# Optimization experiments

Hardware: AMD Instinct MI355X
Metric: run time of the kernel (lower is better)

Reference implementation:

```python
import jax, jax.numpy as jnp
import numpy as np

EMB = 1024
HEADS = 16
HEADSIZE = EMB // HEADS
EPS = 1e-5  # torch LayerNorm default


def _layernorm(x, g, b):
    # normalize over last dim (headsize)
    m = jnp.mean(x, axis=-1, keepdims=True)
    v = jnp.mean((x - m) ** 2, axis=-1, keepdims=True)
    return (x - m) * jax.lax.rsqrt(v + EPS) * g + b


def setup_inputs() -> dict:
    key = jax.random.key(0)
    ks = jax.random.split(key, 6)
    B, T = 4, 2048
    s = 1.0 / np.sqrt(EMB)  # ~ torch Linear init scale
    return {
        "x": jax.random.normal(ks[0], (B, T, EMB), dtype=jnp.float32),
        "Wk": jax.random.normal(ks[1], (EMB, EMB), dtype=jnp.float32) * s,
        "Wq": jax.random.normal(ks[2], (EMB, EMB), dtype=jnp.float32) * s,
        "Wv": jax.random.normal(ks[3], (EMB, EMB), dtype=jnp.float32) * s,
        "Wo": jax.random.normal(ks[4], (EMB, EMB), dtype=jnp.float32) * s,
        "bo": jnp.zeros((EMB,), dtype=jnp.float32),
        "kln_g": jnp.ones((HEADSIZE,), dtype=jnp.float32),
        "kln_b": jnp.zeros((HEADSIZE,), dtype=jnp.float32),
        "qln_g": jnp.ones((HEADSIZE,), dtype=jnp.float32),
        "qln_b": jnp.zeros((HEADSIZE,), dtype=jnp.float32),
    }


def reference(x, Wk, Wq, Wv, Wo, bo, kln_g, kln_b, qln_g, qln_b):
    B, T, E = x.shape
    # projections (torch Linear: y = x @ W.T), split into heads
    k = jnp.einsum("bte,fe->btf", x, Wk).reshape(B, T, HEADS, HEADSIZE)
    q = jnp.einsum("bte,fe->btf", x, Wq).reshape(B, T, HEADS, HEADSIZE)
    v = jnp.einsum("bte,fe->btf", x, Wv).reshape(B, T, HEADS, HEADSIZE)
    # optional per-head layernorm on keys/queries (kqnorm=True)
    k = _layernorm(k, kln_g, kln_b)
    q = _layernorm(q, qln_g, qln_b)
    # note: original scales by emb**-1/4 on each of q and k (total 1/sqrt(emb))
    scale = E ** (-0.25)
    q = q * scale
    k = k * scale
    # full [B, H, T, T] score matrix (faithful to bmm implementation)
    dot = jnp.einsum("bihd,bjhd->bhij", q, k)
    # causal mask: j > i set to -inf (mask_diagonal=False -> offset=1)
    causal = jnp.triu(jnp.ones((T, T), dtype=bool), k=1)
    dot = jnp.where(causal, -jnp.inf, dot)
    att = jax.nn.softmax(dot, axis=-1)
    out = jnp.einsum("bhij,bjhd->bihd", att, v).reshape(B, T, E)
    return jnp.einsum("bte,fe->btf", out, Wo) + bo
```

## Files before the change

### kernel.cpp

```cpp
#include <hip/hip_runtime.h>
#include <hip/hip_bf16.h>
#include <cstdint>

#define EMB 1024
#define HEADS 16
#define HD 64
#define BATCH 4
#define SEQ 2048
#define BT (BATCH*SEQ)
#define LNEPS 1e-5f
#define QK_SCALE 0.17677669529663687f
#define LOG2E 1.4426950408889634f

typedef __bf16 bf16;
typedef __bf16 bf16x8 __attribute__((ext_vector_type(8)));
typedef __bf16 bf16x4 __attribute__((ext_vector_type(4)));
typedef float  f32x4  __attribute__((ext_vector_type(4)));
typedef short  s16x4  __attribute__((ext_vector_type(4)));

typedef const __attribute__((address_space(1))) void* gas_ptr;
typedef __attribute__((address_space(3))) void*       las_ptr;

__device__ __forceinline__ void gld_lds16(const void* g, void* l) {
  __builtin_amdgcn_global_load_lds((gas_ptr)g, (las_ptr)l, 16, 0, 0);
}

__device__ __forceinline__ f32x4 mfma_pv(bf16x4 a, bf16x4 b, f32x4 c) {
  return __builtin_amdgcn_mfma_f32_16x16x16bf16_1k(
      __builtin_bit_cast(s16x4, a), __builtin_bit_cast(s16x4, b), c, 0, 0, 0);
}

__global__ void cvt_f32_bf16(const float* __restrict__ src, bf16* __restrict__ dst, int n4) {
  int i = blockIdx.x * blockDim.x + threadIdx.x;
  if (i >= n4) return;
  float4 f = reinterpret_cast<const float4*>(src)[i];
  bf16x4 o = { (bf16)f.x, (bf16)f.y, (bf16)f.z, (bf16)f.w };
  reinterpret_cast<bf16x4*>(dst)[i] = o;
}

__global__ void cvt_w4(const float* __restrict__ w0, const float* __restrict__ w1,
                       const float* __restrict__ w2, const float* __restrict__ w3,
                       bf16* __restrict__ dst) {
  int i = blockIdx.x * blockDim.x + threadIdx.x;
  int sel = i >> 18;
  int j = i & 262143;
  const float* s = (sel == 0) ? w0 : (sel == 1) ? w1 : (sel == 2) ? w2 : w3;
  float4 f = reinterpret_cast<const float4*>(s)[j];
  bf16x4 o = { (bf16)f.x, (bf16)f.y, (bf16)f.z, (bf16)f.w };
  reinterpret_cast<bf16x4*>(dst)[i] = o;
}

template<int OUTF32>
__global__ __launch_bounds__(256, 2) void gemm_bt(
    const bf16* __restrict__ A, const bf16* __restrict__ Bm,
    bf16* __restrict__ Cb, float* __restrict__ Cf, const float* __restrict__ bias,
    int M, int N, int K)
{
  __shared__ __align__(16) bf16 As[128 * 32];
  __shared__ __align__(16) bf16 Bs[128 * 32];

  const int t    = threadIdx.x;
  const int lane = t & 63;
  const int wave = t >> 6;
  const int q    = lane >> 4;
  const int ln   = lane & 15;
  const int m0   = blockIdx.y * 128;
  const int n0   = blockIdx.x * 128;
  const int wm   = (wave >> 1) * 64;
  const int wn   = (wave & 1) * 64;

  const int r0 = t >> 2;
  const int c0 = (t & 3) << 3;

  f32x4 zero4 = {0.f, 0.f, 0.f, 0.f};
  f32x4 acc[4][4];
#pragma unroll
  for (int i = 0; i < 4; i++)
#pragma unroll
    for (int j = 0; j < 4; j++) acc[i][j] = zero4;

  for (int k0 = 0; k0 < K; k0 += 32) {
    __syncthreads();
    const bf16* ga = A  + (size_t)(m0 + r0) * K + k0 + c0;
    const bf16* gb = Bm + (size_t)(n0 + r0) * K + k0 + c0;
    gld_lds16(ga,                  &As[t * 8]);
    gld_lds16(ga + (size_t)64 * K, &As[t * 8 + 2048]);
    gld_lds16(gb,                  &Bs[t * 8]);
    gld_lds16(gb + (size_t)64 * K, &Bs[t * 8 + 2048]);
    __syncthreads();

    bf16x8 af[4], bfr[4];
#pragma unroll
    for (int mi = 0; mi < 4; mi++)
      af[mi] = *reinterpret_cast<const bf16x8*>(&As[(wm + mi * 16 + ln) * 32 + q * 8]);
#pragma unroll
    for (int ni = 0; ni < 4; ni++)
      bfr[ni] = *reinterpret_cast<const bf16x8*>(&Bs[(wn + ni * 16 + ln) * 32 + q * 8]);
#pragma unroll
    for (int mi = 0; mi < 4; mi++)
#pragma unroll
      for (int ni = 0; ni < 4; ni++)
        acc[mi][ni] = __builtin_amdgcn_mfma_f32_16x16x32_bf16(af[mi], bfr[ni], acc[mi][ni], 0, 0, 0);
  }

#pragma unroll
  for (int mi = 0; mi < 4; mi++) {
#pragma unroll
    for (int ni = 0; ni < 4; ni++) {
#pragma unroll
      for (int r = 0; r < 4; r++) {
        int row = m0 + wm + mi * 16 + q * 4 + r;
        int col = n0 + wn + ni * 16 + ln;
        float v = acc[mi][ni][r];
        if (OUTF32) Cf[(size_t)row * N + col] = v + bias[col];
        else        Cb[(size_t)row * N + col] = (bf16)v;
      }
    }
  }
}

__global__ void ln_kq(const bf16* __restrict__ kqv,
                      bf16* __restrict__ kn, bf16* __restrict__ qn,
                      const float* __restrict__ kg, const float* __restrict__ kb,
                      const float* __restrict__ qg, const float* __restrict__ qb,
                      float kscale, float qscale)
{
  const int t = threadIdx.x;
  const int lr = t & 7;
  const int row = blockIdx.x * 32 + (t >> 3);
  const int tok = row >> 4, h = row & 15;
  const size_t base = (size_t)tok * (3 * EMB) + h * HD + lr * 8;

  bf16x8 vk = *reinterpret_cast<const bf16x8*>(kqv + base);
  bf16x8 vq = *reinterpret_cast<const bf16x8*>(kqv + base + EMB);

  float fk[8], fq[8];
  float sk = 0.f, sq = 0.f, s2k = 0.f, s2q = 0.f;
#pragma unroll
  for (int e = 0; e < 8; e++) {
    fk[e] = (float)vk[e]; fq[e] = (float)vq[e];
    sk += fk[e]; sq += fq[e];
    s2k += fk[e] * fk[e]; s2q += fq[e] * fq[e];
  }
#pragma unroll
  for (int m = 1; m < 8; m <<= 1) {
    sk  += __shfl_xor(sk,  m, 64); sq  += __shfl_xor(sq,  m, 64);
    s2k += __shfl_xor(s2k, m, 64); s2q += __shfl_xor(s2q, m, 64);
  }
  float mk = sk * (1.f / 64.f), mq = sq * (1.f / 64.f);
  float rk = rsqrtf(s2k * (1.f / 64.f) - mk * mk + LNEPS) * kscale;
  float rq = rsqrtf(s2q * (1.f / 64.f) - mq * mq + LNEPS) * qscale;

  bf16x8 ok, oq;
#pragma unroll
  for (int e = 0; e < 8; e++) {
    float gk = kg[lr * 8 + e], bk2 = kb[lr * 8 + e];
    float gq = qg[lr * 8 + e], bq2 = qb[lr * 8 + e];
    ok[e] = (bf16)(((fk[e] - mk) * rk) * gk + bk2 * kscale);
    oq[e] = (bf16)(((fq[e] - mq) * rq) * gq + bq2 * qscale);
  }
  const int b = tok >> 11, tt = tok & 2047;
  const size_t o = ((size_t)(b * HEADS + h) * SEQ + tt) * HD + lr * 8;
  *reinterpret_cast<bf16x8*>(kn + o) = ok;
  *reinterpret_cast<bf16x8*>(qn + o) = oq;
}

__global__ void v_trans(const bf16* __restrict__ in, int ldin, bf16* __restrict__ out)
{
  __shared__ __align__(16) bf16 tile[64][72];
  int bh = blockIdx.y, jt = blockIdx.x;
  int b = bh >> 4, h = bh & 15;
  int t = threadIdx.x;
#pragma unroll
  for (int p = 0; p < 2; p++) {
    int rowj = p * 32 + (t >> 3);
    int cold = (t & 7) << 3;
    bf16x8 v = *reinterpret_cast<const bf16x8*>(
        &in[(size_t)(b * SEQ + jt * 64 + rowj) * ldin + h * HD + cold]);
    *reinterpret_cast<bf16x8*>(&tile[rowj][cold]) = v;
  }
  __syncthreads();
#pragma unroll
  for (int p = 0; p < 2; p++) {
    int rowd = p * 32 + (t >> 3);
    int colj = (t & 7) << 3;
    bf16x8 v;
#pragma unroll
    for (int jj = 0; jj < 8; jj++) v[jj] = tile[colj + jj][rowd];
    *reinterpret_cast<bf16x8*>(&out[((size_t)bh * HD + rowd) * SEQ + jt * 64 + colj]) = v;
  }
}

__global__ __launch_bounds__(256, 4) void attn(
    const bf16* __restrict__ Qn, const bf16* __restrict__ Kn, const bf16* __restrict__ Vt,
    bf16* __restrict__ O)
{
  __shared__ __align__(16) bf16 Ks[2][64 * 64];
  __shared__ __align__(16) bf16 Vs[2][64 * 64];

  const int id = blockIdx.x;
  const int bh = ((id >> 7) << 3) | (id & 7);
  const int bxi = (id >> 3) & 15;
  const int t = threadIdx.x, wave = t >> 6, lane = t & 63;
  const int q = lane >> 4, ln = lane & 15;
  const int b = bh >> 4, h = bh & 15;

  const int u0 = t * 8, u1 = t * 8 + 2048;
  const int kr0 = u0 >> 6, kc0 = ((u0 >> 3) & 7) ^ (kr0 & 7);
  const int kr1 = u1 >> 6, kc1 = ((u1 >> 3) & 7) ^ (kr1 & 7);
  const int vd0 = u0 >> 6, vc0 = ((u0 >> 3) & 7) ^ (vd0 & 7);
  const int vd1 = u1 >> 6, vc1 = ((u1 >> 3) & 7) ^ (vd1 & 7);
  const bf16* Kb = Kn + (size_t)bh * SEQ * HD;
  const bf16* Vb = Vt + (size_t)bh * HD * SEQ;

  f32x4 zero4 = {0.f, 0.f, 0.f, 0.f};

  for (int pass = 0; pass < 2; ++pass) {
    const int itile = pass ? (31 - bxi) : bxi;
    const int qbase = itile * 64 + wave * 16;

    const bf16* qp = Qn + ((size_t)bh * SEQ + qbase + ln) * HD + q * 8;
    bf16x8 qf0 = *reinterpret_cast<const bf16x8*>(qp);
    bf16x8 qf1 = *reinterpret_cast<const bf16x8*>(qp + 32);

    float lrow = 0.f;
    f32x4 oacc[4];
#pragma unroll
    for (int md = 0; md < 4; md++) oacc[md] = zero4;

    const int nj = itile + 1;

    __syncthreads();
    {
      gld_lds16(Kb + (size_t)kr0 * HD + kc0 * 8, &Ks[0][u0]);
      gld_lds16(Kb + (size_t)kr1 * HD + kc1 * 8, &Ks[0][u1]);
      gld_lds16(Vb + (size_t)vd0 * SEQ + vc0 * 8, &Vs[0][u0]);
      gld_lds16(Vb + (size_t)vd1 * SEQ + vc1 * 8, &Vs[0][u1]);
    }

    for (int jt = 0; jt < nj; ++jt) {
      const int buf = jt & 1;
      const int j0 = jt * 64;
      __syncthreads();
      if (jt + 1 < nj) {
        const int jn = j0 + 64;
        gld_lds16(Kb + (size_t)(jn + kr0) * HD + kc0 * 8, &Ks[buf ^ 1][u0]);
        gld_lds16(Kb + (size_t)(jn + kr1) * HD + kc1 * 8, &Ks[buf ^ 1][u1]);
        gld_lds16(Vb + (size_t)vd0 * SEQ + jn + vc0 * 8, &Vs[buf ^ 1][u0]);
        gld_lds16(Vb + (size_t)vd1 * SEQ + jn + vc1 * 8, &Vs[buf ^ 1][u1]);
      }

#pragma unroll
      for (int jb = 0; jb < 4; ++jb) {
        const int jslab = j0 + jb * 16;
        if (jslab <= qbase + 15) {
          const int rowj = jb * 16 + ln;
          bf16x8 kf0 = *reinterpret_cast<const bf16x8*>(
              &Ks[buf][rowj * 64 + ((q)     ^ (rowj & 7)) * 8]);
          bf16x8 kf1 = *reinterpret_cast<const bf16x8*>(
              &Ks[buf][rowj * 64 + ((4 + q) ^ (rowj & 7)) * 8]);
          f32x4 z = zero4;
          z = __builtin_amdgcn_mfma_f32_16x16x32_bf16(kf0, qf0, z, 0, 0, 0);
          z = __builtin_amdgcn_mfma_f32_16x16x32_bf16(kf1, qf1, z, 0, 0, 0);
          if (jslab + 15 > qbase) {
#pragma unroll
            for (int r = 0; r < 4; r++) {
              int jj = jslab + q * 4 + r;
              int ii = qbase + ln;
              if (jj > ii) z[r] = -1.0e30f;
            }
          }
          float p0 = exp2f(z[0]), p1 = exp2f(z[1]), p2 = exp2f(z[2]), p3 = exp2f(z[3]);
          lrow += (p0 + p1) + (p2 + p3);
          bf16x4 pk = { (bf16)p0, (bf16)p1, (bf16)p2, (bf16)p3 };

#pragma unroll
          for (int md = 0; md < 4; md++) {
            const int rowd = md * 16 + ln;
            const bf16* vp = &Vs[buf][rowd * 64 +
                (((jb * 2 + (q >> 1)) ^ (rowd & 7)) * 8) + (q & 1) * 4];
            bf16x4 vf = *reinterpret_cast<const bf16x4*>(vp);
            oacc[md] = mfma_pv(vf, pk, oacc[md]);
          }
        }
      }
    }

    float s = lrow;
    s += __shfl_xor(s, 16, 64);
    s += __shfl_xor(s, 32, 64);
    const float inv = 1.f / s;
    const int row = qbase + ln;
#pragma unroll
    for (int md = 0; md < 4; md++) {
      bf16x4 o4 = { (bf16)(oacc[md][0] * inv), (bf16)(oacc[md][1] * inv),
                    (bf16)(oacc[md][2] * inv), (bf16)(oacc[md][3] * inv) };
      int col = h * HD + md * 16 + q * 4;
      *reinterpret_cast<bf16x4*>(&O[(size_t)(b * SEQ + row) * EMB + col]) = o4;
    }
  }
}

extern "C" void kernel_launch(void* const* d_in, const int* in_sizes, int n_in,
                              void* d_out, int out_size, void* d_ws, size_t ws_size,
                              hipStream_t stream)
{
  const float* x   = (const float*)d_in[0];
  const float* Wk  = (const float*)d_in[1];
  const float* Wq  = (const float*)d_in[2];
  const float* Wv  = (const float*)d_in[3];
  const float* Wo  = (const float*)d_in[4];
  const float* bo  = (const float*)d_in[5];
  const float* klg = (const float*)d_in[6];
  const float* klb = (const float*)d_in[7];
  const float* qlg = (const float*)d_in[8];
  const float* qlb = (const float*)d_in[9];
  float* out = (float*)d_out;

  char* ws = (char*)d_ws;
  const size_t OFF_XB  = 0;
  const size_t OFF_WB  = OFF_XB  + (size_t)BT * EMB * 2;
  const size_t OFF_KQV = OFF_WB  + (size_t)4 * EMB * EMB * 2;
  const size_t OFF_KN  = OFF_KQV + (size_t)BT * 3 * EMB * 2;
  const size_t OFF_QN  = OFF_KN  + (size_t)BT * EMB * 2;
  const size_t OFF_VT  = OFF_QN  + (size_t)BT * EMB * 2;
  const size_t OFF_END = OFF_VT  + (size_t)BT * EMB * 2;
  if (ws_size < OFF_END) return;

  bf16* xb   = (bf16*)(ws + OFF_XB);
  bf16* wb   = (bf16*)(ws + OFF_WB);
  bf16* kqv  = (bf16*)(ws + OFF_KQV);
  bf16* kn   = (bf16*)(ws + OFF_KN);
  bf16* qn   = (bf16*)(ws + OFF_QN);
  bf16* vt   = (bf16*)(ws + OFF_VT);
  bf16* ob   = (bf16*)(ws + OFF_KQV);

  cvt_f32_bf16<<<(BT * EMB / 4) / 256, 256, 0, stream>>>(x, xb, BT * EMB / 4);
  cvt_w4<<<(4 * EMB * EMB / 4) / 256, 256, 0, stream>>>(Wk, Wq, Wv, Wo, wb);

  gemm_bt<0><<<dim3(3 * EMB / 128, BT / 128), 256, 0, stream>>>(
      xb, wb, kqv, (float*)nullptr, (const float*)nullptr, BT, 3 * EMB, EMB);

  ln_kq<<<BT * HEADS / 32, 256, 0, stream>>>(kqv, kn, qn, klg, klb, qlg, qlb,
                                             QK_SCALE * LOG2E, QK_SCALE);
  v_trans<<<dim3(SEQ / 64, BATCH * HEADS), 256, 0, stream>>>(kqv + 2 * EMB, 3 * EMB, vt);

  attn<<<dim3(16 * BATCH * HEADS), 256, 0, stream>>>(qn, kn, vt, ob);

  gemm_bt<1><<<dim3(EMB / 128, BT / 128), 256, 0, stream>>>(
      ob, wb + (size_t)3 * EMB * EMB, (bf16*)nullptr, out, bo, BT, EMB, EMB);
}
```

Measured before the change: 291.5 us.

## Process paired causal query tiles in one KV sweep sharing K/V loads

The attention kernel used to run two separate passes over the key/value tiles, one per paired query tile (bxi and 31-bxi). It now keeps both query tiles' accumulators live and streams K/V once up to the longer tile, computing the short tile only while jt <= iA. This roughly halves the K/V global-to-LDS traffic and barrier count for the short tile and gives more independent MFMA work per loaded tile. In exchange it holds more registers (two accumulator sets and two Q fragments), which could affect occupancy under launch_bounds(256,4).

Measured after the change: 288.9 us. Within noise of the previous version (-0.9%).

```diff
diff --git a/kernel.cpp b/kernel.cpp
--- a/kernel.cpp
+++ b/kernel.cpp
@@ -205,6 +205,11 @@
   const int q = lane >> 4, ln = lane & 15;
   const int b = bh >> 4, h = bh & 15;
 
+  const int iA = bxi;
+  const int iB = 31 - bxi;
+  const int qbaseA = iA * 64 + wave * 16;
+  const int qbaseB = iB * 64 + wave * 16;
+
   const int u0 = t * 8, u1 = t * 8 + 2048;
   const int kr0 = u0 >> 6, kc0 = ((u0 >> 3) & 7) ^ (kr0 & 7);
   const int kr1 = u1 >> 6, kc1 = ((u1 >> 3) & 7) ^ (kr1 & 7);
@@ -215,82 +220,95 @@
 
   f32x4 zero4 = {0.f, 0.f, 0.f, 0.f};
 
-  for (int pass = 0; pass < 2; ++pass) {
-    const int itile = pass ? (31 - bxi) : bxi;
-    const int qbase = itile * 64 + wave * 16;
-
-    const bf16* qp = Qn + ((size_t)bh * SEQ + qbase + ln) * HD + q * 8;
-    bf16x8 qf0 = *reinterpret_cast<const bf16x8*>(qp);
-    bf16x8 qf1 = *reinterpret_cast<const bf16x8*>(qp + 32);
-
-    float lrow = 0.f;
-    f32x4 oacc[4];
-#pragma unroll
-    for (int md = 0; md < 4; md++) oacc[md] = zero4;
-
-    const int nj = itile + 1;
-
-    __syncthreads();
-    {
-      gld_lds16(Kb + (size_t)kr0 * HD + kc0 * 8, &Ks[0][u0]);
-      gld_lds16(Kb + (size_t)kr1 * HD + kc1 * 8, &Ks[0][u1]);
-      gld_lds16(Vb + (size_t)vd0 * SEQ + vc0 * 8, &Vs[0][u0]);
-      gld_lds16(Vb + (size_t)vd1 * SEQ + vc1 * 8, &Vs[0][u1]);
-    }
-
-    for (int jt = 0; jt < nj; ++jt) {
-      const int buf = jt & 1;
-      const int j0 = jt * 64;
-      __syncthreads();
-      if (jt + 1 < nj) {
-        const int jn = j0 + 64;
-        gld_lds16(Kb + (size_t)(jn + kr0) * HD + kc0 * 8, &Ks[buf ^ 1][u0]);
-        gld_lds16(Kb + (size_t)(jn + kr1) * HD + kc1 * 8, &Ks[buf ^ 1][u1]);
-        gld_lds16(Vb + (size_t)vd0 * SEQ + jn + vc0 * 8, &Vs[buf ^ 1][u0]);
-        gld_lds16(Vb + (size_t)vd1 * SEQ + jn + vc1 * 8, &Vs[buf ^ 1][u1]);
-      }
-
-#pragma unroll
-      for (int jb = 0; jb < 4; ++jb) {
-        const int jslab = j0 + jb * 16;
-        if (jslab <= qbase + 15) {
-          const int rowj = jb * 16 + ln;
-          bf16x8 kf0 = *reinterpret_cast<const bf16x8*>(
-              &Ks[buf][rowj * 64 + ((q)     ^ (rowj & 7)) * 8]);
-          bf16x8 kf1 = *reinterpret_cast<const bf16x8*>(
-              &Ks[buf][rowj * 64 + ((4 + q) ^ (rowj & 7)) * 8]);
-          f32x4 z = zero4;
-          z = __builtin_amdgcn_mfma_f32_16x16x32_bf16(kf0, qf0, z, 0, 0, 0);
-          z = __builtin_amdgcn_mfma_f32_16x16x32_bf16(kf1, qf1, z, 0, 0, 0);
-          if (jslab + 15 > qbase) {
-#pragma unroll
-            for (int r = 0; r < 4; r++) {
-              int jj = jslab + q * 4 + r;
-              int ii = qbase + ln;
-              if (jj > ii) z[r] = -1.0e30f;
-            }
-          }
-          float p0 = exp2f(z[0]), p1 = exp2f(z[1]), p2 = exp2f(z[2]), p3 = exp2f(z[3]);
-          lrow += (p0 + p1) + (p2 + p3);
-          bf16x4 pk = { (bf16)p0, (bf16)p1, (bf16)p2, (bf16)p3 };
-
-#pragma unroll
-          for (int md = 0; md < 4; md++) {
-            const int rowd = md * 16 + ln;
-            const bf16* vp = &Vs[buf][rowd * 64 +
-                (((jb * 2 + (q >> 1)) ^ (rowd & 7)) * 8) + (q & 1) * 4];
-            bf16x4 vf = *reinterpret_cast<const bf16x4*>(vp);
-            oacc[md] = mfma_pv(vf, pk, oacc[md]);
-          }
+  const bf16* qpA = Qn + ((size_t)bh * SEQ + qbaseA + ln) * HD + q * 8;
+  const bf16* qpB = Qn + ((size_t)bh * SEQ + qbaseB + ln) * HD + q * 8;
+  bf16x8 qfA0 = *reinterpret_cast<const bf16x8*>(qpA);
+  bf16x8 qfA1 = *reinterpret_cast<const bf16x8*>(qpA + 32);
+  bf16x8 qfB0 = *reinterpret_cast<const bf16x8*>(qpB);
+  bf16x8 qfB1 = *reinterpret_cast<const bf16x8*>(qpB + 32);
+
+  float lrowA = 0.f, lrowB = 0.f;
+  f32x4 oaccA[4], oaccB[4];
+#pragma unroll
+  for (int md = 0; md < 4; md++) { oaccA[md] = zero4; oaccB[md] = zero4; }
+
+  auto slab = [&](int jslab, int jb, int buf, int qbase,
+                  const bf16x8& qf0, const bf16x8& qf1,
+                  f32x4* oacc, float& lrow) {
+    if (jslab <= qbase + 15) {
+      const int rowj = jb * 16 + ln;
+      bf16x8 kf0 = *reinterpret_cast<const bf16x8*>(
+          &Ks[buf][rowj * 64 + ((q)     ^ (rowj & 7)) * 8]);
+      bf16x8 kf1 = *reinterpret_cast<const bf16x8*>(
+          &Ks[buf][rowj * 64 + ((4 + q) ^ (rowj & 7)) * 8]);
+      f32x4 z = zero4;
+      z = __builtin_amdgcn_mfma_f32_16x16x32_bf16(kf0, qf0, z, 0, 0, 0);
+      z = __builtin_amdgcn_mfma_f32_16x16x32_bf16(kf1, qf1, z, 0, 0, 0);
+      if (jslab + 15 > qbase) {
+#pragma unroll
+        for (int r = 0; r < 4; r++) {
+          int jj = jslab + q * 4 + r;
+          int ii = qbase + ln;
+          if (jj > ii) z[r] = -1.0e30f;
         }
       }
-    }
-
-    float s = lrow;
+      float p0 = exp2f(z[0]), p1 = exp2f(z[1]), p2 = exp2f(z[2]), p3 = exp2f(z[3]);
+      lrow += (p0 + p1) + (p2 + p3);
+      bf16x4 pk = { (bf16)p0, (bf16)p1, (bf16)p2, (bf16)p3 };
+
+#pragma unroll
+      for (int md = 0; md < 4; md++) {
+        const int rowd = md * 16 + ln;
+        const bf16* vp = &Vs[buf][rowd * 64 +
+            (((jb * 2 + (q >> 1)) ^ (rowd & 7)) * 8) + (q & 1) * 4];
+        bf16x4 vf = *reinterpret_cast<const bf16x4*>(vp);
+        oacc[md] = mfma_pv(vf, pk, oacc[md]);
+      }
+    }
+  };
+
+  const int nj = iB + 1;
+
+  {
+    gld_lds16(Kb + (size_t)kr0 * HD + kc0 * 8, &Ks[0][u0]);
+    gld_lds16(Kb + (size_t)kr1 * HD + kc1 * 8, &Ks[0][u1]);
+    gld_lds16(Vb + (size_t)vd0 * SEQ + vc0 * 8, &Vs[0][u0]);
+    gld_lds16(Vb + (size_t)vd1 * SEQ + vc1 * 8, &Vs[0][u1]);
+  }
+
+  for (int jt = 0; jt < nj; ++jt) {
+    const int buf = jt & 1;
+    const int j0 = jt * 64;
+    __syncthreads();
+    if (jt + 1 < nj) {
+      const int jn = j0 + 64;
+      gld_lds16(Kb + (size_t)(jn + kr0) * HD + kc0 * 8, &Ks[buf ^ 1][u0]);
+      gld_lds16(Kb + (size_t)(jn + kr1) * HD + kc1 * 8, &Ks[buf ^ 1][u1]);
+      gld_lds16(Vb + (size_t)vd0 * SEQ + jn + vc0 * 8, &Vs[buf ^ 1][u0]);
+      gld_lds16(Vb + (size_t)vd1 * SEQ + jn + vc1 * 8, &Vs[buf ^ 1][u1]);
+    }
+
+    if (jt <= iA) {
+#pragma unroll
+      for (int jb = 0; jb < 4; ++jb)
+        slab(j0 + jb * 16, jb, buf, qbaseA, qfA0, qfA1, oaccA, lrowA);
+    }
+    {
+#pragma unroll
+      for (int jb = 0; jb < 4; ++jb)
+        slab(j0 + jb * 16, jb, buf, qbaseB, qfB0, qfB1, oaccB, lrowB);
+    }
+  }
+
+#pragma unroll
+  for (int sidx = 0; sidx < 2; ++sidx) {
+    float s = sidx ? lrowB : lrowA;
+    f32x4* oacc = sidx ? oaccB : oaccA;
+    const int qb = sidx ? qbaseB : qbaseA;
     s += __shfl_xor(s, 16, 64);
     s += __shfl_xor(s, 32, 64);
     const float inv = 1.f / s;
-    const int row = qbase + ln;
+    const int row = qb + ln;
 #pragma unroll
     for (int md = 0; md < 4; md++) {
       bf16x4 o4 = { (bf16)(oacc[md][0] * inv), (bf16)(oacc[md][1] * inv),
```

## Merge conversion and LN/transpose launches, remap GEMM blocks across XCDs

Applied to the files above, without the earlier changes.

Folds the x and weight fp32-to-bf16 conversions into one launch, and the K/Q layernorm with the V transpose into another, removing two kernel launches and their inter-kernel gaps. The GEMM now remaps its linear block id so that consecutive blocks landing on the same XCD share a group of M rows, aiming for better L2 reuse of A tiles. The remap assumes gridDim.y == 64 and gridDim.x a multiple of 8, which holds for both GEMM calls here.

Result: faster. 279.8 us (-4.0%).

```diff
diff --git a/kernel.cpp b/kernel.cpp
--- a/kernel.cpp
+++ b/kernel.cpp
@@ -30,24 +30,25 @@
       __builtin_bit_cast(s16x4, a), __builtin_bit_cast(s16x4, b), c, 0, 0, 0);
 }
 
-__global__ void cvt_f32_bf16(const float* __restrict__ src, bf16* __restrict__ dst, int n4) {
-  int i = blockIdx.x * blockDim.x + threadIdx.x;
-  if (i >= n4) return;
-  float4 f = reinterpret_cast<const float4*>(src)[i];
-  bf16x4 o = { (bf16)f.x, (bf16)f.y, (bf16)f.z, (bf16)f.w };
-  reinterpret_cast<bf16x4*>(dst)[i] = o;
-}
-
-__global__ void cvt_w4(const float* __restrict__ w0, const float* __restrict__ w1,
-                       const float* __restrict__ w2, const float* __restrict__ w3,
-                       bf16* __restrict__ dst) {
-  int i = blockIdx.x * blockDim.x + threadIdx.x;
-  int sel = i >> 18;
-  int j = i & 262143;
-  const float* s = (sel == 0) ? w0 : (sel == 1) ? w1 : (sel == 2) ? w2 : w3;
-  float4 f = reinterpret_cast<const float4*>(s)[j];
-  bf16x4 o = { (bf16)f.x, (bf16)f.y, (bf16)f.z, (bf16)f.w };
-  reinterpret_cast<bf16x4*>(dst)[i] = o;
+__global__ void cvt_all(const float* __restrict__ x,
+                        const float* __restrict__ w0, const float* __restrict__ w1,
+                        const float* __restrict__ w2, const float* __restrict__ w3,
+                        bf16* __restrict__ xb, bf16* __restrict__ wb) {
+  const int bid = blockIdx.x;
+  if (bid < 8192) {
+    int i = bid * 256 + threadIdx.x;
+    float4 f = reinterpret_cast<const float4*>(x)[i];
+    bf16x4 o = { (bf16)f.x, (bf16)f.y, (bf16)f.z, (bf16)f.w };
+    reinterpret_cast<bf16x4*>(xb)[i] = o;
+  } else {
+    int i = (bid - 8192) * 256 + threadIdx.x;
+    int sel = i >> 18;
+    int j = i & 262143;
+    const float* s = (sel == 0) ? w0 : (sel == 1) ? w1 : (sel == 2) ? w2 : w3;
+    float4 f = reinterpret_cast<const float4*>(s)[j];
+    bf16x4 o = { (bf16)f.x, (bf16)f.y, (bf16)f.z, (bf16)f.w };
+    reinterpret_cast<bf16x4*>(wb)[i] = o;
+  }
 }
 
 template<int OUTF32>
@@ -64,8 +65,15 @@
   const int wave = t >> 6;
   const int q    = lane >> 4;
   const int ln   = lane & 15;
-  const int m0   = blockIdx.y * 128;
-  const int n0   = blockIdx.x * 128;
+
+  const int lid = (int)blockIdx.y * (int)gridDim.x + (int)blockIdx.x;
+  const int xcd = lid & 7;
+  const int nn  = lid >> 3;
+  const int bxr = nn >> 3;
+  const int byr = (xcd << 3) | (nn & 7);
+  const int m0  = byr * 128;
+  const int n0  = bxr * 128;
+
   const int wm   = (wave >> 1) * 64;
   const int wn   = (wave & 1) * 64;
 
@@ -119,75 +127,77 @@
   }
 }
 
-__global__ void ln_kq(const bf16* __restrict__ kqv,
+__global__ void ln_vt(const bf16* __restrict__ kqv,
                       bf16* __restrict__ kn, bf16* __restrict__ qn,
+                      bf16* __restrict__ vt,
                       const float* __restrict__ kg, const float* __restrict__ kb,
                       const float* __restrict__ qg, const float* __restrict__ qb,
                       float kscale, float qscale)
 {
+  __shared__ __align__(16) bf16 tile[64][72];
+  const int bid = blockIdx.x;
   const int t = threadIdx.x;
-  const int lr = t & 7;
-  const int row = blockIdx.x * 32 + (t >> 3);
-  const int tok = row >> 4, h = row & 15;
-  const size_t base = (size_t)tok * (3 * EMB) + h * HD + lr * 8;
-
-  bf16x8 vk = *reinterpret_cast<const bf16x8*>(kqv + base);
-  bf16x8 vq = *reinterpret_cast<const bf16x8*>(kqv + base + EMB);
-
-  float fk[8], fq[8];
-  float sk = 0.f, sq = 0.f, s2k = 0.f, s2q = 0.f;
-#pragma unroll
-  for (int e = 0; e < 8; e++) {
-    fk[e] = (float)vk[e]; fq[e] = (float)vq[e];
-    sk += fk[e]; sq += fq[e];
-    s2k += fk[e] * fk[e]; s2q += fq[e] * fq[e];
-  }
-#pragma unroll
-  for (int m = 1; m < 8; m <<= 1) {
-    sk  += __shfl_xor(sk,  m, 64); sq  += __shfl_xor(sq,  m, 64);
-    s2k += __shfl_xor(s2k, m, 64); s2q += __shfl_xor(s2q, m, 64);
-  }
-  float mk = sk * (1.f / 64.f), mq = sq * (1.f / 64.f);
-  float rk = rsqrtf(s2k * (1.f / 64.f) - mk * mk + LNEPS) * kscale;
-  float rq = rsqrtf(s2q * (1.f / 64.f) - mq * mq + LNEPS) * qscale;
-
-  bf16x8 ok, oq;
-#pragma unroll
-  for (int e = 0; e < 8; e++) {
-    float gk = kg[lr * 8 + e], bk2 = kb[lr * 8 + e];
-    float gq = qg[lr * 8 + e], bq2 = qb[lr * 8 + e];
-    ok[e] = (bf16)(((fk[e] - mk) * rk) * gk + bk2 * kscale);
-    oq[e] = (bf16)(((fq[e] - mq) * rq) * gq + bq2 * qscale);
-  }
-  const int b = tok >> 11, tt = tok & 2047;
-  const size_t o = ((size_t)(b * HEADS + h) * SEQ + tt) * HD + lr * 8;
-  *reinterpret_cast<bf16x8*>(kn + o) = ok;
-  *reinterpret_cast<bf16x8*>(qn + o) = oq;
-}
-
-__global__ void v_trans(const bf16* __restrict__ in, int ldin, bf16* __restrict__ out)
-{
-  __shared__ __align__(16) bf16 tile[64][72];
-  int bh = blockIdx.y, jt = blockIdx.x;
-  int b = bh >> 4, h = bh & 15;
-  int t = threadIdx.x;
-#pragma unroll
-  for (int p = 0; p < 2; p++) {
-    int rowj = p * 32 + (t >> 3);
-    int cold = (t & 7) << 3;
-    bf16x8 v = *reinterpret_cast<const bf16x8*>(
-        &in[(size_t)(b * SEQ + jt * 64 + rowj) * ldin + h * HD + cold]);
-    *reinterpret_cast<bf16x8*>(&tile[rowj][cold]) = v;
-  }
-  __syncthreads();
-#pragma unroll
-  for (int p = 0; p < 2; p++) {
-    int rowd = p * 32 + (t >> 3);
-    int colj = (t & 7) << 3;
-    bf16x8 v;
-#pragma unroll
-    for (int jj = 0; jj < 8; jj++) v[jj] = tile[colj + jj][rowd];
-    *reinterpret_cast<bf16x8*>(&out[((size_t)bh * HD + rowd) * SEQ + jt * 64 + colj]) = v;
+  if (bid < 4096) {
+    const int lr = t & 7;
+    const int row = bid * 32 + (t >> 3);
+    const int tok = row >> 4, h = row & 15;
+    const size_t base = (size_t)tok * (3 * EMB) + h * HD + lr * 8;
+
+    bf16x8 vk = *reinterpret_cast<const bf16x8*>(kqv + base);
+    bf16x8 vq = *reinterpret_cast<const bf16x8*>(kqv + base + EMB);
+
+    float fk[8], fq[8];
+    float sk = 0.f, sq = 0.f, s2k = 0.f, s2q = 0.f;
+#pragma unroll
+    for (int e = 0; e < 8; e++) {
+      fk[e] = (float)vk[e]; fq[e] = (float)vq[e];
+      sk += fk[e]; sq += fq[e];
+      s2k += fk[e] * fk[e]; s2q += fq[e] * fq[e];
+    }
+#pragma unroll
+    for (int m = 1; m < 8; m <<= 1) {
+      sk  += __shfl_xor(sk,  m, 64); sq  += __shfl_xor(sq,  m, 64);
+      s2k += __shfl_xor(s2k, m, 64); s2q += __shfl_xor(s2q, m, 64);
+    }
+    float mk = sk * (1.f / 64.f), mq = sq * (1.f / 64.f);
+    float rk = rsqrtf(s2k * (1.f / 64.f) - mk * mk + LNEPS) * kscale;
+    float rq = rsqrtf(s2q * (1.f / 64.f) - mq * mq + LNEPS) * qscale;
+
+    bf16x8 ok, oq;
+#pragma unroll
+    for (int e = 0; e < 8; e++) {
+      float gk = kg[lr * 8 + e], bk2 = kb[lr * 8 + e];
+      float gq = qg[lr * 8 + e], bq2 = qb[lr * 8 + e];
+      ok[e] = (bf16)(((fk[e] - mk) * rk) * gk + bk2 * kscale);
+      oq[e] = (bf16)(((fq[e] - mq) * rq) * gq + bq2 * qscale);
+    }
+    const int b = tok >> 11, tt = tok & 2047;
+    const size_t o = ((size_t)(b * HEADS + h) * SEQ + tt) * HD + lr * 8;
+    *reinterpret_cast<bf16x8*>(kn + o) = ok;
+    *reinterpret_cast<bf16x8*>(qn + o) = oq;
+  } else {
+    const int idx = bid - 4096;
+    const int jt = idx & 31, bh = idx >> 5;
+    const int b = bh >> 4, h = bh & 15;
+    const bf16* in = kqv + 2 * EMB;
+#pragma unroll
+    for (int p = 0; p < 2; p++) {
+      int rowj = p * 32 + (t >> 3);
+      int cold = (t & 7) << 3;
+      bf16x8 v = *reinterpret_cast<const bf16x8*>(
+          &in[(size_t)(b * SEQ + jt * 64 + rowj) * (3 * EMB) + h * HD + cold]);
+      *reinterpret_cast<bf16x8*>(&tile[rowj][cold]) = v;
+    }
+    __syncthreads();
+#pragma unroll
+    for (int p = 0; p < 2; p++) {
+      int rowd = p * 32 + (t >> 3);
+      int colj = (t & 7) << 3;
+      bf16x8 v;
+#pragma unroll
+      for (int jj = 0; jj < 8; jj++) v[jj] = tile[colj + jj][rowd];
+      *reinterpret_cast<bf16x8*>(&vt[((size_t)bh * HD + rowd) * SEQ + jt * 64 + colj]) = v;
+    }
   }
 }
 
@@ -335,15 +345,13 @@
   bf16* vt   = (bf16*)(ws + OFF_VT);
   bf16* ob   = (bf16*)(ws + OFF_KQV);
 
-  cvt_f32_bf16<<<(BT * EMB / 4) / 256, 256, 0, stream>>>(x, xb, BT * EMB / 4);
-  cvt_w4<<<(4 * EMB * EMB / 4) / 256, 256, 0, stream>>>(Wk, Wq, Wv, Wo, wb);
+  cvt_all<<<12288, 256, 0, stream>>>(x, Wk, Wq, Wv, Wo, xb, wb);
 
   gemm_bt<0><<<dim3(3 * EMB / 128, BT / 128), 256, 0, stream>>>(
       xb, wb, kqv, (float*)nullptr, (const float*)nullptr, BT, 3 * EMB, EMB);
 
-  ln_kq<<<BT * HEADS / 32, 256, 0, stream>>>(kqv, kn, qn, klg, klb, qlg, qlb,
-                                             QK_SCALE * LOG2E, QK_SCALE);
-  v_trans<<<dim3(SEQ / 64, BATCH * HEADS), 256, 0, stream>>>(kqv + 2 * EMB, 3 * EMB, vt);
+  ln_vt<<<4096 + 2048, 256, 0, stream>>>(kqv, kn, qn, vt, klg, klb, qlg, qlb,
+                                         QK_SCALE * LOG2E, QK_SCALE);
 
   attn<<<dim3(16 * BATCH * HEADS), 256, 0, stream>>>(qn, kn, vt, ob);
 
```
